# Kernel tuning notes

Measured on AMD Instinct MI355X. Metric: run time of the kernel, lower is better.

## Reference

```python
import jax, jax.numpy as jnp
import numpy as np

E, H, I, K = 8, 1024, 768, 2
T = 2048  # flattened batch*seq tokens

def setup_inputs() -> dict:
    key = jax.random.key(0)
    k1, k2, k3, k4, k5 = jax.random.split(key, 5)
    hidden_states = jax.random.normal(k1, (T, H), dtype=jnp.float32)
    gate_up_proj = jax.random.normal(k2, (E, 2 * I, H), dtype=jnp.float32) * 0.02
    down_proj = jax.random.normal(k3, (E, H, I), dtype=jnp.float32) * 0.02
    top_k_index = jax.random.randint(k4, (T, K), 0, E)
    top_k_weights = jax.nn.softmax(jax.random.normal(k5, (T, K), dtype=jnp.float32), axis=-1)
    return {
        "hidden_states": hidden_states,
        "gate_up_proj": gate_up_proj,
        "down_proj": down_proj,
        "top_k_index": top_k_index,
        "top_k_weights": top_k_weights,
    }


def reference(hidden_states, gate_up_proj, down_proj, top_k_index, top_k_weights):
    # hidden_states: [T, H]; gate_up_proj: [E, 2I, H]; down_proj: [E, H, I]
    # top_k_index: [T, K] int; top_k_weights: [T, K] float
    num_experts = gate_up_proj.shape[0]
    # Combine weights per (token, expert): zero for unrouted experts, so the
    # dense-over-experts compute below yields exactly the routed MoE output.
    onehot = jax.nn.one_hot(top_k_index, num_experts, dtype=hidden_states.dtype)  # [T, K, E]
    combine = jnp.einsum("tke,tk->te", onehot, top_k_weights)  # [T, E]
    # Grouped GEMM 1: fused gate+up projection for all experts.
    gu = jnp.einsum("th,eoh->teo", hidden_states, gate_up_proj)  # [T, E, 2I]
    inter = gu.shape[-1] // 2
    gate, up = gu[..., :inter], gu[..., inter:]
    h = jax.nn.silu(gate) * up  # [T, E, I]
    # Grouped GEMM 2: down projection.
    expert_out = jnp.einsum("tei,ehi->teh", h, down_proj)  # [T, E, H]
    return jnp.einsum("teh,te->th", expert_out, combine)  # [T, H]
```

## Files before the change

kernel.cpp:

```cpp
#include <hip/hip_runtime.h>
#include <hip/hip_bf16.h>

#define T_TOK   2048
#define NEXP    8
#define HDIM    1024
#define IDIM    768
#define TOPK    2
#define NASSIGN (T_TOK*TOPK)
#define MT      64
#define MAX_TILES 72
#define SLOT_PAD 4224

typedef unsigned short u16;
typedef unsigned int   u32;

typedef __bf16 bf16x8 __attribute__((ext_vector_type(8)));
typedef float  f32x4  __attribute__((ext_vector_type(4)));

struct Meta {
  int n_tiles;
  int _pad[15];
  int tile_e[80];
  int tile_m[80];
  int tile_n[80];
};

__device__ __forceinline__ u16 f2bf(float f) {
  u32 x = __float_as_uint(f);
  return (u16)((x + 0x7fffu + ((x >> 16) & 1u)) >> 16);
}

__device__ __forceinline__ int4 pack8(const float* __restrict__ p) {
  float4 a = *(const float4*)p;
  float4 b = *(const float4*)(p + 4);
  union { u16 u[8]; int4 v; } r;
  r.u[0] = f2bf(a.x); r.u[1] = f2bf(a.y); r.u[2] = f2bf(a.z); r.u[3] = f2bf(a.w);
  r.u[4] = f2bf(b.x); r.u[5] = f2bf(b.y); r.u[6] = f2bf(b.z); r.u[7] = f2bf(b.w);
  return r.v;
}

__device__ __forceinline__ bf16x8 asbf(int4 v) {
  return __builtin_bit_cast(bf16x8, v);
}

__global__ void route_k(const int* __restrict__ topk, const float* __restrict__ tw,
                        Meta* __restrict__ meta, int* __restrict__ slot_token,
                        float* __restrict__ slot_w) {
  __shared__ int s_cnt[NEXP], s_off[NEXP], s_cur[NEXP];
  int tid = threadIdx.x;
  if (tid < NEXP) { s_cnt[tid] = 0; s_cur[tid] = 0; }
  __syncthreads();
  for (int i = tid; i < NASSIGN; i += blockDim.x)
    atomicAdd(&s_cnt[topk[i]], 1);
  __syncthreads();
  if (tid == 0) {
    int acc = 0, nt = 0;
    for (int e = 0; e < NEXP; ++e) {
      s_off[e] = acc;
      int c = s_cnt[e];
      for (int mb = 0; mb < c; mb += MT) {
        meta->tile_e[nt] = e;
        meta->tile_m[nt] = acc + mb;
        meta->tile_n[nt] = (c - mb) < MT ? (c - mb) : MT;
        ++nt;
      }
      acc += c;
    }
    meta->n_tiles = nt;
  }
  __syncthreads();
  for (int i = tid; i < NASSIGN; i += blockDim.x) {
    int e = topk[i];
    int p = s_off[e] + atomicAdd(&s_cur[e], 1);
    slot_token[p] = i / TOPK;
    slot_w[p]     = tw[i];
  }
}

__global__ void cvt_k(const float* __restrict__ src, u16* __restrict__ dst, int n) {
  int i = (blockIdx.x * blockDim.x + threadIdx.x) * 4;
  if (i >= n) return;
  float4 f = *(const float4*)(src + i);
  ushort4 o;
  o.x = f2bf(f.x); o.y = f2bf(f.y); o.z = f2bf(f.z); o.w = f2bf(f.w);
  *(ushort4*)(dst + i) = o;
}

__global__ void cvt8_k(const float* __restrict__ src, u16* __restrict__ dst, int n8) {
  int i = blockIdx.x * blockDim.x + threadIdx.x;
  if (i >= n8) return;
  *(int4*)(dst + (size_t)i * 8) = pack8(src + (size_t)i * 8);
}

__global__ __launch_bounds__(256) void gemm1_k(
    const u16* __restrict__ hs16, const u16* __restrict__ gup16,
    const Meta* __restrict__ meta, const int* __restrict__ slot_token,
    const float* __restrict__ slot_w, u16* __restrict__ hbuf) {
  int tile = blockIdx.x;
  if (tile >= meta->n_tiles) return;
  int e = meta->tile_e[tile], mbase = meta->tile_m[tile], nrows = meta->tile_n[tile];
  int n0 = blockIdx.y * 64;

  __shared__ int4 As[512], Bg[512], Bu[512];
  int tid = threadIdx.x;
  int lane = tid & 63, w = tid >> 6, wm = w >> 1, wn = w & 1;
  f32x4 accg[2][2] = {}; f32x4 accu[2][2] = {};
  const size_t wbase = (size_t)e * (2 * IDIM) * HDIM;

  for (int k0 = 0; k0 < HDIM; k0 += 64) {
    __syncthreads();
    #pragma unroll
    for (int c = tid; c < 512; c += 256) {
      int row = c >> 3, slot = c & 7;
      int4 v = {0, 0, 0, 0};
      if (row < nrows) {
        int tok = slot_token[mbase + row];
        v = *(const int4*)(hs16 + (size_t)tok * HDIM + k0 + slot * 8);
      }
      As[(row << 3) | (slot ^ (row & 7))] = v;
    }
    #pragma unroll
    for (int c = tid; c < 512; c += 256) {
      int row = c >> 3, slot = c & 7;
      const u16* pg = gup16 + wbase + (size_t)(n0 + row) * HDIM + k0 + slot * 8;
      int idx = (row << 3) | (slot ^ (row & 7));
      Bg[idx] = *(const int4*)pg;
      Bu[idx] = *(const int4*)(pg + (size_t)IDIM * HDIM);
    }
    __syncthreads();
    #pragma unroll
    for (int ks = 0; ks < 2; ++ks) {
      bf16x8 af[2], bgf[2], buf_[2];
      int slot = ks * 4 + (lane >> 4);
      #pragma unroll
      for (int i = 0; i < 2; ++i) {
        int row = wm * 32 + i * 16 + (lane & 15);
        af[i] = asbf(As[(row << 3) | (slot ^ (row & 7))]);
      }
      #pragma unroll
      for (int j = 0; j < 2; ++j) {
        int row = wn * 32 + j * 16 + (lane & 15);
        int idx = (row << 3) | (slot ^ (row & 7));
        bgf[j]  = asbf(Bg[idx]);
        buf_[j] = asbf(Bu[idx]);
      }
      #pragma unroll
      for (int i = 0; i < 2; ++i)
        #pragma unroll
        for (int j = 0; j < 2; ++j) {
          accg[i][j] = __builtin_amdgcn_mfma_f32_16x16x32_bf16(af[i], bgf[j],  accg[i][j], 0, 0, 0);
          accu[i][j] = __builtin_amdgcn_mfma_f32_16x16x32_bf16(af[i], buf_[j], accu[i][j], 0, 0, 0);
        }
    }
  }

  int fq = lane >> 4, fr = lane & 15;
  #pragma unroll
  for (int i = 0; i < 2; ++i)
    #pragma unroll
    for (int r = 0; r < 4; ++r) {
      int row = wm * 32 + i * 16 + fq * 4 + r;
      if (row < nrows) {
        float wgt = slot_w[mbase + row];
        #pragma unroll
        for (int j = 0; j < 2; ++j) {
          float g = accg[i][j][r], u = accu[i][j][r];
          float s = g / (1.0f + __expf(-g));
          hbuf[(size_t)(mbase + row) * IDIM + n0 + wn * 32 + j * 16 + fr] = f2bf(s * u * wgt);
        }
      }
    }
}

__global__ __launch_bounds__(256) void gemm2_k(
    const u16* __restrict__ hbuf, const u16* __restrict__ down16,
    const Meta* __restrict__ meta, const int* __restrict__ slot_token,
    float* __restrict__ out) {
  int tile = blockIdx.x;
  if (tile >= meta->n_tiles) return;
  int e = meta->tile_e[tile], mbase = meta->tile_m[tile], nrows = meta->tile_n[tile];
  int n0 = blockIdx.y * 64;

  __shared__ int4 As[512], Bs[512];
  int tid = threadIdx.x;
  int lane = tid & 63, w = tid >> 6, wm = w >> 1, wn = w & 1;
  f32x4 acc[2][2] = {};
  const size_t dbase = (size_t)e * HDIM * IDIM;

  for (int k0 = 0; k0 < IDIM; k0 += 64) {
    __syncthreads();
    #pragma unroll
    for (int c = tid; c < 512; c += 256) {
      int row = c >> 3, slot = c & 7;
      As[(row << 3) | (slot ^ (row & 7))] =
          *(const int4*)(hbuf + (size_t)(mbase + row) * IDIM + k0 + slot * 8);
    }
    #pragma unroll
    for (int c = tid; c < 512; c += 256) {
      int row = c >> 3, slot = c & 7;
      Bs[(row << 3) | (slot ^ (row & 7))] =
          *(const int4*)(down16 + dbase + (size_t)(n0 + row) * IDIM + k0 + slot * 8);
    }
    __syncthreads();
    #pragma unroll
    for (int ks = 0; ks < 2; ++ks) {
      bf16x8 af[2], bf[2];
      int slot = ks * 4 + (lane >> 4);
      #pragma unroll
      for (int i = 0; i < 2; ++i) {
        int row = wm * 32 + i * 16 + (lane & 15);
        af[i] = asbf(As[(row << 3) | (slot ^ (row & 7))]);
      }
      #pragma unroll
      for (int j = 0; j < 2; ++j) {
        int row = wn * 32 + j * 16 + (lane & 15);
        bf[j] = asbf(Bs[(row << 3) | (slot ^ (row & 7))]);
      }
      #pragma unroll
      for (int i = 0; i < 2; ++i)
        #pragma unroll
        for (int j = 0; j < 2; ++j)
          acc[i][j] = __builtin_amdgcn_mfma_f32_16x16x32_bf16(af[i], bf[j], acc[i][j], 0, 0, 0);
    }
  }

  int fq = lane >> 4, fr = lane & 15;
  #pragma unroll
  for (int i = 0; i < 2; ++i)
    #pragma unroll
    for (int r = 0; r < 4; ++r) {
      int row = wm * 32 + i * 16 + fq * 4 + r;
      if (row < nrows) {
        int tok = slot_token[mbase + row];
        #pragma unroll
        for (int j = 0; j < 2; ++j)
          atomicAdd(out + (size_t)tok * HDIM + n0 + wn * 32 + j * 16 + fr, acc[i][j][r]);
      }
    }
}

extern "C" void kernel_launch(void* const* d_in, const int* in_sizes, int n_in,
                              void* d_out, int out_size, void* d_ws, size_t ws_size,
                              hipStream_t stream) {
  const float* hs   = (const float*)d_in[0];
  const float* gup  = (const float*)d_in[1];
  const float* down = (const float*)d_in[2];
  const int*   topk = (const int*)d_in[3];
  const float* tw   = (const float*)d_in[4];
  float* out = (float*)d_out;

  const size_t o_hs16   = 65536;
  const size_t o_hbuf   = o_hs16   + (size_t)T_TOK * HDIM * 2;
  const size_t o_gup16  = o_hbuf   + (size_t)SLOT_PAD * IDIM * 2;
  const size_t o_down16 = o_gup16  + (size_t)NEXP * 2 * IDIM * HDIM * 2;
  const size_t needed   = o_down16 + (size_t)NEXP * HDIM * IDIM * 2;

  char* ws = (char*)d_ws;
  Meta*  meta       = (Meta*)ws;
  int*   slot_token = (int*)(ws + 4096);
  float* slot_w     = (float*)(ws + 4096 + SLOT_PAD * 4);
  u16*   hs16       = (u16*)(ws + o_hs16);
  u16*   hbuf       = (u16*)(ws + o_hbuf);
  u16*   gup16      = (u16*)(ws + o_gup16);
  u16*   down16     = (u16*)(ws + o_down16);

  if (ws_size < needed) return;

  hipMemsetAsync(d_out, 0, (size_t)out_size * sizeof(float), stream);
  route_k<<<1, 256, 0, stream>>>(topk, tw, meta, slot_token, slot_w);
  cvt_k<<<(T_TOK * HDIM / 4 + 255) / 256, 256, 0, stream>>>(hs, hs16, T_TOK * HDIM);
  {
    int n8g = NEXP * 2 * IDIM * HDIM / 8;
    int n8d = NEXP * HDIM * IDIM / 8;
    cvt8_k<<<(n8g + 255) / 256, 256, 0, stream>>>(gup,  gup16,  n8g);
    cvt8_k<<<(n8d + 255) / 256, 256, 0, stream>>>(down, down16, n8d);
  }
  gemm1_k<<<dim3(MAX_TILES, IDIM / 64), 256, 0, stream>>>(hs16, gup16, meta, slot_token, slot_w, hbuf);
  gemm2_k<<<dim3(MAX_TILES, HDIM / 64), 256, 0, stream>>>(hbuf, down16, meta, slot_token, out);
}
```

Measured before the change: 218.8 us.

## Fuse prep kernels and double-buffer GEMMs with direct global-to-LDS loads

Merges routing, all fp32-to-bf16 conversions and output zeroing into one grid-stride prep kernel, replacing several launches and a memset. Both GEMM kernels now stage tiles through double-buffered LDS using global_load_lds, overlapping the next k-tile fetch with MFMA work and removing one barrier per iteration. Blocks are remapped over a 1D grid with an XCD-aware swizzle and launch bounds allow 3 blocks per CU. Padded slots are zero-filled so partial tiles read valid tokens, which replaces the per-row bounds check in the A load.

```diff
diff --git a/kernel.cpp b/kernel.cpp
--- a/kernel.cpp
+++ b/kernel.cpp
@@ -9,7 +9,7 @@
 #define NASSIGN (T_TOK*TOPK)
 #define MT      64
 #define MAX_TILES 72
-#define SLOT_PAD 4224
+#define SLOT_PAD 4608
 
 typedef unsigned short u16;
 typedef unsigned int   u32;
@@ -43,91 +43,120 @@
   return __builtin_bit_cast(bf16x8, v);
 }
 
-__global__ void route_k(const int* __restrict__ topk, const float* __restrict__ tw,
-                        Meta* __restrict__ meta, int* __restrict__ slot_token,
-                        float* __restrict__ slot_w) {
-  __shared__ int s_cnt[NEXP], s_off[NEXP], s_cur[NEXP];
+__device__ __forceinline__ void gll(const void* g, void* l) {
+  __builtin_amdgcn_global_load_lds(
+      (const __attribute__((address_space(1))) u32*)g,
+      (__attribute__((address_space(3))) u32*)l, 16, 0, 0);
+}
+
+__global__ __launch_bounds__(256) void prep_k(
+    const float* __restrict__ hs, const float* __restrict__ gup,
+    const float* __restrict__ down, const int* __restrict__ topk,
+    const float* __restrict__ tw,
+    u16* __restrict__ hs16, u16* __restrict__ gup16, u16* __restrict__ down16,
+    Meta* __restrict__ meta, int* __restrict__ slot_token, float* __restrict__ slot_w,
+    float* __restrict__ out) {
   int tid = threadIdx.x;
-  if (tid < NEXP) { s_cnt[tid] = 0; s_cur[tid] = 0; }
-  __syncthreads();
-  for (int i = tid; i < NASSIGN; i += blockDim.x)
-    atomicAdd(&s_cnt[topk[i]], 1);
-  __syncthreads();
-  if (tid == 0) {
-    int acc = 0, nt = 0;
-    for (int e = 0; e < NEXP; ++e) {
-      s_off[e] = acc;
-      int c = s_cnt[e];
-      for (int mb = 0; mb < c; mb += MT) {
-        meta->tile_e[nt] = e;
-        meta->tile_m[nt] = acc + mb;
-        meta->tile_n[nt] = (c - mb) < MT ? (c - mb) : MT;
-        ++nt;
-      }
-      acc += c;
-    }
-    meta->n_tiles = nt;
+
+  if (blockIdx.x == 0) {
+    __shared__ int s_cnt[NEXP], s_off[NEXP], s_cur[NEXP];
+    if (tid < NEXP) { s_cnt[tid] = 0; s_cur[tid] = 0; }
+    __syncthreads();
+    for (int i = tid; i < NASSIGN; i += 256)
+      atomicAdd(&s_cnt[topk[i]], 1);
+    __syncthreads();
+    if (tid == 0) {
+      int acc = 0, nt = 0;
+      for (int e = 0; e < NEXP; ++e) {
+        s_off[e] = acc;
+        int c = s_cnt[e];
+        for (int mb = 0; mb < c; mb += MT) {
+          meta->tile_e[nt] = e;
+          meta->tile_m[nt] = acc + mb;
+          meta->tile_n[nt] = (c - mb) < MT ? (c - mb) : MT;
+          ++nt;
+        }
+        acc += c;
+      }
+      meta->n_tiles = nt;
+    }
+    __syncthreads();
+    for (int i = tid; i < NASSIGN; i += 256) {
+      int e = topk[i];
+      int p = s_off[e] + atomicAdd(&s_cur[e], 1);
+      slot_token[p] = i / TOPK;
+      slot_w[p]     = tw[i];
+    }
+    for (int i = NASSIGN + tid; i < SLOT_PAD; i += 256) {
+      slot_token[i] = 0;
+      slot_w[i]     = 0.0f;
+    }
   }
-  __syncthreads();
-  for (int i = tid; i < NASSIGN; i += blockDim.x) {
-    int e = topk[i];
-    int p = s_off[e] + atomicAdd(&s_cur[e], 1);
-    slot_token[p] = i / TOPK;
-    slot_w[p]     = tw[i];
+
+  const size_t NG_GUP = (size_t)NEXP * 2 * IDIM * HDIM / 8;
+  const size_t NG_DWN = (size_t)NEXP * HDIM * IDIM / 8;
+  const size_t NG_HS  = (size_t)T_TOK * HDIM / 8;
+  const size_t NG_OUT = (size_t)T_TOK * HDIM / 4;
+  const size_t TOT = NG_GUP + NG_DWN + NG_HS + NG_OUT;
+  for (size_t g = (size_t)blockIdx.x * 256 + tid; g < TOT; g += (size_t)gridDim.x * 256) {
+    if (g < NG_GUP) {
+      *(int4*)(gup16 + g * 8) = pack8(gup + g * 8);
+    } else if (g < NG_GUP + NG_DWN) {
+      size_t i = g - NG_GUP;
+      *(int4*)(down16 + i * 8) = pack8(down + i * 8);
+    } else if (g < NG_GUP + NG_DWN + NG_HS) {
+      size_t i = g - NG_GUP - NG_DWN;
+      *(int4*)(hs16 + i * 8) = pack8(hs + i * 8);
+    } else {
+      size_t i = g - NG_GUP - NG_DWN - NG_HS;
+      int4 z = {0, 0, 0, 0};
+      *(int4*)(out + i * 4) = z;
+    }
   }
 }
 
-__global__ void cvt_k(const float* __restrict__ src, u16* __restrict__ dst, int n) {
-  int i = (blockIdx.x * blockDim.x + threadIdx.x) * 4;
-  if (i >= n) return;
-  float4 f = *(const float4*)(src + i);
-  ushort4 o;
-  o.x = f2bf(f.x); o.y = f2bf(f.y); o.z = f2bf(f.z); o.w = f2bf(f.w);
-  *(ushort4*)(dst + i) = o;
-}
-
-__global__ void cvt8_k(const float* __restrict__ src, u16* __restrict__ dst, int n8) {
-  int i = blockIdx.x * blockDim.x + threadIdx.x;
-  if (i >= n8) return;
-  *(int4*)(dst + (size_t)i * 8) = pack8(src + (size_t)i * 8);
-}
-
-__global__ __launch_bounds__(256) void gemm1_k(
+__global__ __launch_bounds__(256, 3) void gemm1_k(
     const u16* __restrict__ hs16, const u16* __restrict__ gup16,
     const Meta* __restrict__ meta, const int* __restrict__ slot_token,
     const float* __restrict__ slot_w, u16* __restrict__ hbuf) {
-  int tile = blockIdx.x;
+  int bid = blockIdx.x;
+  int wg = (bid & 7) * 108 + (bid >> 3);
+  int tile = wg / 12, y = wg % 12;
   if (tile >= meta->n_tiles) return;
   int e = meta->tile_e[tile], mbase = meta->tile_m[tile], nrows = meta->tile_n[tile];
-  int n0 = blockIdx.y * 64;
-
-  __shared__ int4 As[512], Bg[512], Bu[512];
-  int tid = threadIdx.x;
-  int lane = tid & 63, w = tid >> 6, wm = w >> 1, wn = w & 1;
-  f32x4 accg[2][2] = {}; f32x4 accu[2][2] = {};
-  const size_t wbase = (size_t)e * (2 * IDIM) * HDIM;
-
+  int n0 = y * 64;
+
+  __shared__ int4 lds[2][3][512];
+  int tid = threadIdx.x, lane = tid & 63, w = tid >> 6, wm = w >> 1, wn = w & 1;
+  f32x4 accg[2][2] = {}, accu[2][2] = {};
+
+  const u16* gb = gup16 + (size_t)e * (2 * IDIM) * HDIM + (size_t)n0 * HDIM;
+  const u16* ub = gb + (size_t)IDIM * HDIM;
+
+  int c0 = tid, c1 = tid + 256;
+  int r0 = c0 >> 3, s0 = (c0 & 7) ^ (r0 & 7);
+  int r1 = c1 >> 3, s1 = (c1 & 7) ^ (r1 & 7);
+  const u16* a0 = hs16 + (size_t)slot_token[mbase + r0] * HDIM + s0 * 8;
+  const u16* a1 = hs16 + (size_t)slot_token[mbase + r1] * HDIM + s1 * 8;
+  const u16* g0 = gb + (size_t)r0 * HDIM + s0 * 8;
+  const u16* g1 = gb + (size_t)r1 * HDIM + s1 * 8;
+  const u16* u0 = ub + (size_t)r0 * HDIM + s0 * 8;
+  const u16* u1 = ub + (size_t)r1 * HDIM + s1 * 8;
+
+  auto STAGE = [&](int b, int k0) {
+    gll(a0 + k0, &lds[b][0][w * 64]);
+    gll(a1 + k0, &lds[b][0][256 + w * 64]);
+    gll(g0 + k0, &lds[b][1][w * 64]);
+    gll(g1 + k0, &lds[b][1][256 + w * 64]);
+    gll(u0 + k0, &lds[b][2][w * 64]);
+    gll(u1 + k0, &lds[b][2][256 + w * 64]);
+  };
+
+  STAGE(0, 0);
+  __syncthreads();
+  int cur = 0;
   for (int k0 = 0; k0 < HDIM; k0 += 64) {
-    __syncthreads();
-    #pragma unroll
-    for (int c = tid; c < 512; c += 256) {
-      int row = c >> 3, slot = c & 7;
-      int4 v = {0, 0, 0, 0};
-      if (row < nrows) {
-        int tok = slot_token[mbase + row];
-        v = *(const int4*)(hs16 + (size_t)tok * HDIM + k0 + slot * 8);
-      }
-      As[(row << 3) | (slot ^ (row & 7))] = v;
-    }
-    #pragma unroll
-    for (int c = tid; c < 512; c += 256) {
-      int row = c >> 3, slot = c & 7;
-      const u16* pg = gup16 + wbase + (size_t)(n0 + row) * HDIM + k0 + slot * 8;
-      int idx = (row << 3) | (slot ^ (row & 7));
-      Bg[idx] = *(const int4*)pg;
-      Bu[idx] = *(const int4*)(pg + (size_t)IDIM * HDIM);
-    }
-    __syncthreads();
+    if (k0 + 64 < HDIM) STAGE(cur ^ 1, k0 + 64);
     #pragma unroll
     for (int ks = 0; ks < 2; ++ks) {
       bf16x8 af[2], bgf[2], buf_[2];
@@ -135,14 +164,14 @@
       #pragma unroll
       for (int i = 0; i < 2; ++i) {
         int row = wm * 32 + i * 16 + (lane & 15);
-        af[i] = asbf(As[(row << 3) | (slot ^ (row & 7))]);
+        af[i] = asbf(lds[cur][0][(row << 3) | (slot ^ (row & 7))]);
       }
       #pragma unroll
       for (int j = 0; j < 2; ++j) {
         int row = wn * 32 + j * 16 + (lane & 15);
         int idx = (row << 3) | (slot ^ (row & 7));
-        bgf[j]  = asbf(Bg[idx]);
-        buf_[j] = asbf(Bu[idx]);
+        bgf[j]  = asbf(lds[cur][1][idx]);
+        buf_[j] = asbf(lds[cur][2][idx]);
       }
       #pragma unroll
       for (int i = 0; i < 2; ++i)
@@ -152,6 +181,8 @@
           accu[i][j] = __builtin_amdgcn_mfma_f32_16x16x32_bf16(af[i], buf_[j], accu[i][j], 0, 0, 0);
         }
     }
+    __syncthreads();
+    cur ^= 1;
   }
 
   int fq = lane >> 4, fr = lane & 15;
@@ -172,36 +203,42 @@
     }
 }
 
-__global__ __launch_bounds__(256) void gemm2_k(
+__global__ __launch_bounds__(256, 3) void gemm2_k(
     const u16* __restrict__ hbuf, const u16* __restrict__ down16,
     const Meta* __restrict__ meta, const int* __restrict__ slot_token,
     float* __restrict__ out) {
-  int tile = blockIdx.x;
+  int bid = blockIdx.x;
+  int wg = (bid & 7) * 144 + (bid >> 3);
+  int tile = wg / 16, y = wg % 16;
   if (tile >= meta->n_tiles) return;
   int e = meta->tile_e[tile], mbase = meta->tile_m[tile], nrows = meta->tile_n[tile];
-  int n0 = blockIdx.y * 64;
-
-  __shared__ int4 As[512], Bs[512];
-  int tid = threadIdx.x;
-  int lane = tid & 63, w = tid >> 6, wm = w >> 1, wn = w & 1;
+  int n0 = y * 64;
+
+  __shared__ int4 lds[2][2][512];
+  int tid = threadIdx.x, lane = tid & 63, w = tid >> 6, wm = w >> 1, wn = w & 1;
   f32x4 acc[2][2] = {};
-  const size_t dbase = (size_t)e * HDIM * IDIM;
-
+  const u16* db = down16 + (size_t)e * HDIM * IDIM + (size_t)n0 * IDIM;
+
+  int c0 = tid, c1 = tid + 256;
+  int r0 = c0 >> 3, s0 = (c0 & 7) ^ (r0 & 7);
+  int r1 = c1 >> 3, s1 = (c1 & 7) ^ (r1 & 7);
+  const u16* a0 = hbuf + (size_t)(mbase + r0) * IDIM + s0 * 8;
+  const u16* a1 = hbuf + (size_t)(mbase + r1) * IDIM + s1 * 8;
+  const u16* b0 = db + (size_t)r0 * IDIM + s0 * 8;
+  const u16* b1 = db + (size_t)r1 * IDIM + s1 * 8;
+
+  auto STAGE = [&](int b, int k0) {
+    gll(a0 + k0, &lds[b][0][w * 64]);
+    gll(a1 + k0, &lds[b][0][256 + w * 64]);
+    gll(b0 + k0, &lds[b][1][w * 64]);
+    gll(b1 + k0, &lds[b][1][256 + w * 64]);
+  };
+
+  STAGE(0, 0);
+  __syncthreads();
+  int cur = 0;
   for (int k0 = 0; k0 < IDIM; k0 += 64) {
-    __syncthreads();
-    #pragma unroll
-    for (int c = tid; c < 512; c += 256) {
-      int row = c >> 3, slot = c & 7;
-      As[(row << 3) | (slot ^ (row & 7))] =
-          *(const int4*)(hbuf + (size_t)(mbase + row) * IDIM + k0 + slot * 8);
-    }
-    #pragma unroll
-    for (int c = tid; c < 512; c += 256) {
-      int row = c >> 3, slot = c & 7;
-      Bs[(row << 3) | (slot ^ (row & 7))] =
-          *(const int4*)(down16 + dbase + (size_t)(n0 + row) * IDIM + k0 + slot * 8);
-    }
-    __syncthreads();
+    if (k0 + 64 < IDIM) STAGE(cur ^ 1, k0 + 64);
     #pragma unroll
     for (int ks = 0; ks < 2; ++ks) {
       bf16x8 af[2], bf[2];
@@ -209,12 +246,12 @@
       #pragma unroll
       for (int i = 0; i < 2; ++i) {
         int row = wm * 32 + i * 16 + (lane & 15);
-        af[i] = asbf(As[(row << 3) | (slot ^ (row & 7))]);
+        af[i] = asbf(lds[cur][0][(row << 3) | (slot ^ (row & 7))]);
       }
       #pragma unroll
       for (int j = 0; j < 2; ++j) {
         int row = wn * 32 + j * 16 + (lane & 15);
-        bf[j] = asbf(Bs[(row << 3) | (slot ^ (row & 7))]);
+        bf[j] = asbf(lds[cur][1][(row << 3) | (slot ^ (row & 7))]);
       }
       #pragma unroll
       for (int i = 0; i < 2; ++i)
@@ -222,6 +259,8 @@
         for (int j = 0; j < 2; ++j)
           acc[i][j] = __builtin_amdgcn_mfma_f32_16x16x32_bf16(af[i], bf[j], acc[i][j], 0, 0, 0);
     }
+    __syncthreads();
+    cur ^= 1;
   }
 
   int fq = lane >> 4, fr = lane & 15;
@@ -250,15 +289,15 @@
   float* out = (float*)d_out;
 
   const size_t o_hs16   = 65536;
-  const size_t o_hbuf   = o_hs16   + (size_t)T_TOK * HDIM * 2;
-  const size_t o_gup16  = o_hbuf   + (size_t)SLOT_PAD * IDIM * 2;
-  const size_t o_down16 = o_gup16  + (size_t)NEXP * 2 * IDIM * HDIM * 2;
+  const size_t o_hbuf   = o_hs16 + (size_t)T_TOK * HDIM * 2;
+  const size_t o_gup16  = o_hbuf + (size_t)SLOT_PAD * IDIM * 2;
+  const size_t o_down16 = o_gup16 + (size_t)NEXP * 2 * IDIM * HDIM * 2;
   const size_t needed   = o_down16 + (size_t)NEXP * HDIM * IDIM * 2;
 
   char* ws = (char*)d_ws;
   Meta*  meta       = (Meta*)ws;
   int*   slot_token = (int*)(ws + 4096);
-  float* slot_w     = (float*)(ws + 4096 + SLOT_PAD * 4);
+  float* slot_w     = (float*)(ws + 24576);
   u16*   hs16       = (u16*)(ws + o_hs16);
   u16*   hbuf       = (u16*)(ws + o_hbuf);
   u16*   gup16      = (u16*)(ws + o_gup16);
@@ -266,15 +305,8 @@
 
   if (ws_size < needed) return;
 
-  hipMemsetAsync(d_out, 0, (size_t)out_size * sizeof(float), stream);
-  route_k<<<1, 256, 0, stream>>>(topk, tw, meta, slot_token, slot_w);
-  cvt_k<<<(T_TOK * HDIM / 4 + 255) / 256, 256, 0, stream>>>(hs, hs16, T_TOK * HDIM);
-  {
-    int n8g = NEXP * 2 * IDIM * HDIM / 8;
-    int n8d = NEXP * HDIM * IDIM / 8;
-    cvt8_k<<<(n8g + 255) / 256, 256, 0, stream>>>(gup,  gup16,  n8g);
-    cvt8_k<<<(n8d + 255) / 256, 256, 0, stream>>>(down, down16, n8d);
-  }
-  gemm1_k<<<dim3(MAX_TILES, IDIM / 64), 256, 0, stream>>>(hs16, gup16, meta, slot_token, slot_w, hbuf);
-  gemm2_k<<<dim3(MAX_TILES, HDIM / 64), 256, 0, stream>>>(hbuf, down16, meta, slot_token, out);
-}
+  prep_k<<<2048, 256, 0, stream>>>(hs, gup, down, topk, tw,
+                                   hs16, gup16, down16, meta, slot_token, slot_w, out);
+  gemm1_k<<<MAX_TILES * 12, 256, 0, stream>>>(hs16, gup16, meta, slot_token, slot_w, hbuf);
+  gemm2_k<<<MAX_TILES * 16, 256, 0, stream>>>(hbuf, down16, meta, slot_token, out);
+}
```

New measurement: 198.6 us. -9.2%, faster.
